# Performance work log

Hardware: AMD Instinct MI355X
Metric: run time of the kernel (lower is better)

The kernel has to match this reference:

```python
import jax, jax.numpy as jnp
import numpy as np

B, S, R, D, A, P = 64, 128, 8, 10000, 10, 256


def setup_inputs() -> dict:
    key = jax.random.key(0)
    ks = jax.random.split(key, 7)
    return {
        "atom_hvs": jax.random.normal(ks[0], (A, D), jnp.float32),
        "pos_hvs": jax.random.normal(ks[1], (S, D), jnp.float32),
        "closure_tag": jax.random.normal(ks[2], (D,), jnp.float32),
        "W": jax.random.normal(ks[3], (P, D), jnp.float32) / np.float32(np.sqrt(D)),
        "b": jax.random.normal(ks[4], (P,), jnp.float32) * 0.01,
        "token_mask": jnp.ones((B, S), jnp.float32),
        "ring_mask": jnp.ones((B, R), jnp.float32),
        "atom_idx": jax.random.randint(ks[5], (B, S), 0, A),
        "ring_pos": jax.random.randint(ks[6], (B, R, 2), 0, S),
    }


def reference(atom_hvs, pos_hvs, closure_tag, W, b, token_mask, ring_mask, atom_idx, ring_pos):
    # HRR bind = circular convolution -> pointwise multiply in rFFT domain.
    # Bundle = sum; by linearity we sum in the frequency domain and do a
    # single irfft per molecule (same math as per-token conv + add).
    d = atom_hvs.shape[-1]
    Fa = jnp.fft.rfft(atom_hvs, axis=-1)          # [A, F]
    Fp = jnp.fft.rfft(pos_hvs, axis=-1)           # [S, F]
    Fc = jnp.fft.rfft(closure_tag)                # [F]

    s = atom_idx.shape[1]
    tok = Fa[atom_idx] * Fp[None, :s, :]          # [B, S, F] gather+bind
    freq = jnp.sum(token_mask[..., None] * tok, axis=1)   # [B, F] bundle

    ring = Fp[ring_pos[..., 0]] * Fp[ring_pos[..., 1]] * Fc  # [B, R, F]
    freq = freq + jnp.sum(ring_mask[..., None] * ring, axis=1)

    mol_hv = jnp.fft.irfft(freq, n=d, axis=-1)    # [B, D]
    return mol_hv @ W.T + b                       # [B, proj_dim]
```

## Files before the change

kernel.cpp:

```cpp
#include <hip/hip_runtime.h>

#define PI2 6.28318530717958647692f

#define NSIG 139
#define FS   5120

__global__ __launch_bounds__(256) void k_fwd(
                     const float* __restrict__ atom, const float* __restrict__ pos,
                     const float* __restrict__ clo, float2* __restrict__ spec) {
  __shared__ float xs[5000];
  unsigned sig = blockIdx.x, q = blockIdx.y;
  unsigned k1base = q * 10u;
  unsigned nk1 = (k1base + 10u <= 51u) ? 10u : (51u - k1base);
  const float* xb = (sig < 128u) ? (pos + sig * 10000u)
                   : ((sig < 138u) ? (atom + (sig - 128u) * 10000u) : clo);
  int tid = threadIdx.x;
  unsigned ntile1 = nk1 * 25u;
  unsigned k1l = tid / 25u, n2 = (tid % 25u) * 4u;
  bool have = (unsigned)tid < ntile1;
  unsigned k1 = k1base + k1l;
  float cth, sth;
  __sincosf(PI2 * (float)k1 * 0.01f, &sth, &cth);
  float c = 1.0f, s = 0.0f;
  float ar[4] = {}, as[4] = {};

  for (int h = 0; h < 2; ++h) {
    for (int i = tid; i < 1250; i += 256)
      *(float4*)(xs + 4 * i) = *(const float4*)(xb + h * 5000 + 4 * i);
    __syncthreads();
    if (have) {
#pragma unroll 5
      for (int n1l = 0; n1l < 50; ++n1l) {
        const float4 xv = *(const float4*)(xs + n1l * 100 + n2);
        ar[0] += xv.x * c; as[0] += xv.x * s;
        ar[1] += xv.y * c; as[1] += xv.y * s;
        ar[2] += xv.z * c; as[2] += xv.z * s;
        ar[3] += xv.w * c; as[3] += xv.w * s;
        float cn = c * cth - s * sth;
        float sn = s * cth + c * sth;
        c = cn; s = sn;
      }
    }
    __syncthreads();
  }

  if (have) {
    unsigned rb = (100u - k1) % 100u;
    float resA[8], resB[8];
#pragma unroll
    for (int j = 0; j < 4; ++j) {
      float swA, cwA, swB, cwB;
      __sincosf(PI2 * (float)((n2 + j) * k1) * 1e-4f, &swA, &cwA);
      __sincosf(PI2 * (float)((n2 + j) * rb) * 1e-4f, &swB, &cwB);
      resA[2 * j + 0] = ar[j] * cwA - as[j] * swA;
      resA[2 * j + 1] = -(as[j] * cwA + ar[j] * swA);
      resB[2 * j + 0] = ar[j] * cwB + as[j] * swB;
      resB[2 * j + 1] = as[j] * cwB - ar[j] * swB;
    }
    float* pA = xs + k1l * 200u + n2 * 2u;
    float* pB = xs + (nk1 + k1l) * 200u + n2 * 2u;
    *(float4*)(pA + 0) = make_float4(resA[0], resA[1], resA[2], resA[3]);
    *(float4*)(pA + 4) = make_float4(resA[4], resA[5], resA[6], resA[7]);
    *(float4*)(pB + 0) = make_float4(resB[0], resB[1], resB[2], resB[3]);
    *(float4*)(pB + 4) = make_float4(resB[4], resB[5], resB[6], resB[7]);
  }
  __syncthreads();

  unsigned nrow = 2u * nk1;
  unsigned ntile3 = nrow * 26u;
  for (unsigned t = tid; t < ntile3; t += 256u) {
    unsigned lr = t / 26u, k2 = (t % 26u) * 2u;
    unsigned gk1 = (lr < nk1) ? (k1base + lr) : ((100u - (k1base + (lr - nk1))) % 100u);
    const float* brow = xs + lr * 200u;
    float cthA, sthA, cthB, sthB;
    __sincosf(PI2 * (float)k2 * 0.01f, &sthA, &cthA);
    __sincosf(PI2 * (float)(k2 + 1) * 0.01f, &sthB, &cthB);
    float cA = 1.0f, sA = 0.0f, cB = 1.0f, sB = 0.0f;
    float reA = 0.f, imA = 0.f, reB = 0.f, imB = 0.f;
#pragma unroll 4
    for (int n2i = 0; n2i < 100; n2i += 2) {
      const float4 b0 = *(const float4*)(brow + 2 * n2i);
      reA += b0.x * cA + b0.y * sA;  imA += b0.y * cA - b0.x * sA;
      reB += b0.x * cB + b0.y * sB;  imB += b0.y * cB - b0.x * sB;
      float cA1 = cA * cthA - sA * sthA, sA1 = sA * cthA + cA * sthA;
      float cB1 = cB * cthB - sB * sthB, sB1 = sB * cthB + cB * sthB;
      reA += b0.z * cA1 + b0.w * sA1;  imA += b0.w * cA1 - b0.z * sA1;
      reB += b0.z * cB1 + b0.w * sB1;  imB += b0.w * cB1 - b0.z * sB1;
      cA = cA1 * cthA - sA1 * sthA; sA = sA1 * cthA + cA1 * sthA;
      cB = cB1 * cthB - sB1 * sthB; sB = sB1 * cthB + cB1 * sthB;
    }
    unsigned kA = gk1 + 100u * k2;
    unsigned kB = gk1 + 100u * (k2 + 1);
    if (kA <= 5000u) spec[sig * FS + kA] = make_float2(reA, imA);
    if (kB <= 5000u) spec[sig * FS + kB] = make_float2(reB, imB);
  }
}

__global__ __launch_bounds__(256) void k_mix(const float2* __restrict__ spec,
                      const float* __restrict__ tmask, const float* __restrict__ rmask,
                      const int* __restrict__ aidx, const int* __restrict__ rpos,
                      float2* __restrict__ G) {
  __shared__ float2 FaS[10][128];
  __shared__ float2 FcS[128];
  __shared__ float tmS[4][128];
  __shared__ int   aiS[4][128];
  __shared__ float rmS[4][8];
  __shared__ int   rpS[4][8][2];
  __shared__ float2 red[2][4][128];
  int tid = threadIdx.x;
  int kl = tid & 127, half = tid >> 7;
  int k = blockIdx.x * 128 + kl;
  int kc = k > 5000 ? 5000 : k;
  int b0 = blockIdx.y * 4;
  for (int i = tid; i < 10 * 128; i += 256) {
    int a = i >> 7, kk = i & 127;
    int kg = blockIdx.x * 128 + kk; if (kg > 5000) kg = 5000;
    FaS[a][kk] = spec[(128 + a) * FS + kg];
  }
  if (tid < 128) FcS[tid] = spec[138 * FS + kc];
  for (int i = tid; i < 4 * 128; i += 256) {
    int bb = i >> 7, ss = i & 127;
    tmS[bb][ss] = tmask[(b0 + bb) * 128 + ss];
    aiS[bb][ss] = aidx[(b0 + bb) * 128 + ss];
  }
  if (tid < 32) {
    int bb = tid >> 3, rr = tid & 7;
    rmS[bb][rr] = rmask[(b0 + bb) * 8 + rr];
    rpS[bb][rr][0] = rpos[((b0 + bb) * 8 + rr) * 2 + 0];
    rpS[bb][rr][1] = rpos[((b0 + bb) * 8 + rr) * 2 + 1];
  }
  __syncthreads();
  float fr[4] = {}, fi[4] = {};
  int sbase = half * 64;
#pragma unroll 8
  for (int si = 0; si < 64; ++si) {
    int s = sbase + si;
    float2 fp = spec[s * FS + kc];
#pragma unroll
    for (int b = 0; b < 4; ++b) {
      int a = aiS[b][s];
      float tm = tmS[b][s];
      float2 fa = FaS[a][kl];
      fr[b] += tm * (fa.x * fp.x - fa.y * fp.y);
      fi[b] += tm * (fa.x * fp.y + fa.y * fp.x);
    }
  }
  float2 fc = FcS[kl];
#pragma unroll
  for (int rr = 0; rr < 4; ++rr) {
    int r = half * 4 + rr;
#pragma unroll
    for (int b = 0; b < 4; ++b) {
      int p0 = rpS[b][r][0], p1 = rpS[b][r][1];
      float rm = rmS[b][r];
      float2 f0 = spec[p0 * FS + kc];
      float2 f1 = spec[p1 * FS + kc];
      float tr = f0.x * f1.x - f0.y * f1.y;
      float ti = f0.x * f1.y + f0.y * f1.x;
      fr[b] += rm * (tr * fc.x - ti * fc.y);
      fi[b] += rm * (tr * fc.y + ti * fc.x);
    }
  }
#pragma unroll
  for (int b = 0; b < 4; ++b) red[half][b][kl] = make_float2(fr[b], fi[b]);
  __syncthreads();
  if (k <= 5000) {
#pragma unroll
    for (int j = 0; j < 2; ++j) {
      int b = half + 2 * j;
      float R = red[0][b][kl].x + red[1][b][kl].x;
      float I = red[0][b][kl].y + red[1][b][kl].y;
      if (k == 0 || k == 5000) I = 0.0f;
      G[(size_t)(b0 + b) * 10000 + k] = make_float2(R, I);
      if (k >= 1 && k <= 4999)
        G[(size_t)(b0 + b) * 10000 + (10000 - k)] = make_float2(R, -I);
    }
  }
}

__global__ __launch_bounds__(256) void k_i1(const float2* __restrict__ G,
                                            float2* __restrict__ Bi) {
  __shared__ float gs[2600];
  unsigned sig = blockIdx.x;
  const float* gp = (const float*)(G + sig * 10000u);
  int tid = threadIdx.x;
  unsigned t = blockIdx.y * 256u + tid;
  bool have = t < 2600u;
  unsigned m1 = t / 26u, n2 = (t % 26u) * 2u;
  float cth, sth;
  __sincosf(PI2 * (float)m1 * 0.01f, &sth, &cth);
  float reA = 0.f, imA = 0.f, reB = 0.f, imB = 0.f;

  for (int h = 0; h < 4; ++h) {
    if (h) __syncthreads();
    for (int i = tid; i < 650; i += 256) {
      int row = i / 26, c4 = i % 26;
      *(float4*)(gs + row * 104 + c4 * 4) =
          *(const float4*)(gp + (h * 25 + row) * 200 + c4 * 4);
    }
    __syncthreads();
    if (have) {
      unsigned ph = (m1 * (unsigned)h) & 3u;
      float c = (ph == 0u) ? 1.0f : (ph == 2u) ? -1.0f : 0.0f;
      float s = (ph == 1u) ? 1.0f : (ph == 3u) ? -1.0f : 0.0f;
#pragma unroll 5
      for (int n1l = 0; n1l < 25; ++n1l) {
        const float4 gv = *(const float4*)(gs + n1l * 104 + n2 * 2);
        reA += gv.x * c - gv.y * s;  imA += gv.y * c + gv.x * s;
        reB += gv.z * c - gv.w * s;  imB += gv.w * c + gv.z * s;
        float cn = c * cth - s * sth;
        float sn = s * cth + c * sth;
        c = cn; s = sn;
      }
    }
  }
  if (have) {
    float w0 = (n2 == 0u || n2 == 50u) ? 0.5f : 1.0f;
    float w1 = (n2 == 50u) ? 0.0f : 1.0f;
    float sw0, cw0, sw1, cw1;
    __sincosf(PI2 * (float)(n2 * m1) * 1e-4f, &sw0, &cw0);
    __sincosf(PI2 * (float)((n2 + 1u) * m1) * 1e-4f, &sw1, &cw1);
    float4 outv;
    outv.x = (reA * cw0 - imA * sw0) * w0;
    outv.y = (imA * cw0 + reA * sw0) * w0;
    outv.z = (reB * cw1 - imB * sw1) * w1;
    outv.w = (imB * cw1 + reB * sw1) * w1;
    *(float4*)((float*)Bi + (sig * 5200u + m1 * 52u + n2) * 2) = outv;
  }
}

__global__ __launch_bounds__(256) void k_i2(const float2* __restrict__ Bi,
                                            float* __restrict__ mol) {
  __shared__ float bs[2600];
  unsigned sig = blockIdx.x, q = blockIdx.y;
  int tid = threadIdx.x;
  const float* bp = (const float*)Bi + sig * 10400u + q * 2600u;
  for (int i = tid; i < 650; i += 256)
    *(float4*)(bs + 4 * i) = *(const float4*)(bp + 4 * i);
  __syncthreads();
  unsigned t = blockIdx.z * 256u + tid;
  if (t >= 1250u) return;
  unsigned m1l = t / 50u;
  unsigned m2 = (t % 50u) * 2u;
  const float* b0 = bs + m1l * 104u;
  float cthA, sthA, cthB, sthB;
  __sincosf(PI2 * (float)m2 * 0.01f, &sthA, &cthA);
  __sincosf(PI2 * (float)(m2 + 1u) * 0.01f, &sthB, &cthB);
  float cA = 1.0f, sA = 0.0f, cB = 1.0f, sB = 0.0f;
  float r0 = 0.f, r1 = 0.f;
#pragma unroll 4
  for (int jj = 0; jj < 26; ++jj) {
    int n2i = 2 * jj;
    const float4 v0 = *(const float4*)(b0 + 2 * n2i);
    r0 += v0.x * cA - v0.y * sA;
    r1 += v0.x * cB - v0.y * sB;
    float cA1 = cA * cthA - sA * sthA, sA1 = sA * cthA + cA * sthA;
    float cB1 = cB * cthB - sB * sthB, sB1 = sB * cthB + cB * sthB;
    r0 += v0.z * cA1 - v0.w * sA1;
    r1 += v0.z * cB1 - v0.w * sB1;
    cA = cA1 * cthA - sA1 * sthA; sA = sA1 * cthA + cA1 * sthA;
    cB = cB1 * cthB - sB1 * sthB; sB = sB1 * cthB + cB1 * sthB;
  }
  unsigned m1 = q * 25u + m1l;
  mol[sig * 10000u + m1 + 100u * m2] = r0 * 2e-4f;
  mol[sig * 10000u + m1 + 100u * (m2 + 1u)] = r1 * 2e-4f;
}

__global__ __launch_bounds__(512) void k_proj(const float* __restrict__ mol,
                                              const float* __restrict__ W,
                                              float* __restrict__ part) {
  __shared__ float molS[40 * 64];
  int tid = threadIdx.x;
  int d0 = blockIdx.x * 40;
  for (int i = tid; i < 40 * 64; i += 512)
    molS[i] = mol[(size_t)(i & 63) * 10000 + d0 + (i >> 6)];
  __syncthreads();
  int p0 = (tid & 127) * 2;
  int bh = (tid >> 7) * 16;
  float acc[2][16] = {};
  const float* w0 = W + (size_t)(p0 + 0) * 10000 + d0;
  const float* w1 = W + (size_t)(p0 + 1) * 10000 + d0;
#pragma unroll 4
  for (int dl = 0; dl < 40; ++dl) {
    const float wv0 = w0[dl], wv1 = w1[dl];
    const float4* m4 = (const float4*)(molS + dl * 64 + bh);
#pragma unroll
    for (int q = 0; q < 4; ++q) {
      float4 mv = m4[q];
      acc[0][4 * q + 0] += wv0 * mv.x;  acc[1][4 * q + 0] += wv1 * mv.x;
      acc[0][4 * q + 1] += wv0 * mv.y;  acc[1][4 * q + 1] += wv1 * mv.y;
      acc[0][4 * q + 2] += wv0 * mv.z;  acc[1][4 * q + 2] += wv1 * mv.z;
      acc[0][4 * q + 3] += wv0 * mv.w;  acc[1][4 * q + 3] += wv1 * mv.w;
    }
  }
#pragma unroll
  for (int b = 0; b < 16; ++b)
    *(float2*)(part + (size_t)blockIdx.x * 16384 + (bh + b) * 256 + p0) =
        make_float2(acc[0][b], acc[1][b]);
}

__global__ __launch_bounds__(256) void k_red(const float* __restrict__ part,
                                             const float* __restrict__ bias,
                                             float* __restrict__ out) {
  __shared__ float red[4][64];
  int tid = threadIdx.x;
  int pl = tid & 63, cg = tid >> 6;
  int b = blockIdx.x;
  int p = blockIdx.y * 64 + pl;
  float acc = 0.0f;
#pragma unroll 8
  for (int ch = cg; ch < 250; ch += 4)
    acc += part[(size_t)ch * 16384 + b * 256 + p];
  red[cg][pl] = acc;
  __syncthreads();
  if (tid < 64)
    out[b * 256 + p] = red[0][pl] + red[1][pl] + red[2][pl] + red[3][pl] + bias[p];
}

extern "C" void kernel_launch(void* const* d_in, const int* in_sizes, int n_in,
                              void* d_out, int out_size, void* d_ws, size_t ws_size,
                              hipStream_t stream) {
  const float* atom  = (const float*)d_in[0];
  const float* pos   = (const float*)d_in[1];
  const float* clo   = (const float*)d_in[2];
  const float* W     = (const float*)d_in[3];
  const float* bias  = (const float*)d_in[4];
  const float* tmask = (const float*)d_in[5];
  const float* rmask = (const float*)d_in[6];
  const int*   aidx  = (const int*)d_in[7];
  const int*   rpos  = (const int*)d_in[8];
  float* out = (float*)d_out;

  char* ws = (char*)d_ws;
  size_t off = 0;
  auto alloc = [&](size_t n) { off = (off + 255) & ~(size_t)255; size_t o = off; off += n; return o; };
  char* regA   = ws + alloc(16777216);
  float2* Bi   = (float2*)regA;
  float*  part = (float*)regA;
  float2* spec = (float2*)(ws + alloc((size_t)NSIG * FS * 8));
  float2* G    = (float2*)(ws + alloc((size_t)64 * 10000 * 8));
  float*  mol  = (float*)(ws + alloc((size_t)64 * 10000 * 4));

  k_fwd<<<dim3(NSIG, 6), dim3(256), 0, stream>>>(atom, pos, clo, spec);
  k_mix<<<dim3(40, 16), dim3(256), 0, stream>>>(spec, tmask, rmask, aidx, rpos, G);
  k_i1<<<dim3(64, 11), dim3(256), 0, stream>>>(G, Bi);
  k_i2<<<dim3(64, 4, 5), dim3(256), 0, stream>>>(Bi, mol);
  k_proj<<<dim3(250), dim3(512), 0, stream>>>(mol, W, part);
  k_red<<<dim3(64, 4), dim3(256), 0, stream>>>(part, bias, out);
}
```

Before: 188.0 us.

## Drop LDS staging in DFT stages and stage W tile in shared memory for projection

The forward DFT and the two inverse DFT stages now read their inputs straight from global memory instead of first staging them in LDS behind barriers. The aim is to remove the syncthreads and staging overhead and rely on the cache for reuse. The projection kernel now stages the W tile in padded shared memory with coalesced loads and reads mol with a padded stride, replacing strided per-thread global reads of W. This risks more global and L2 traffic in the DFT kernels, and the projection kernel now uses more LDS, which may lower occupancy.

```diff
diff --git a/kernel.cpp b/kernel.cpp
--- a/kernel.cpp
+++ b/kernel.cpp
@@ -8,7 +8,7 @@
 __global__ __launch_bounds__(256) void k_fwd(
                      const float* __restrict__ atom, const float* __restrict__ pos,
                      const float* __restrict__ clo, float2* __restrict__ spec) {
-  __shared__ float xs[5000];
+  __shared__ float xs[4000];
   unsigned sig = blockIdx.x, q = blockIdx.y;
   unsigned k1base = q * 10u;
   unsigned nk1 = (k1base + 10u <= 51u) ? 10u : (51u - k1base);
@@ -24,27 +24,18 @@
   float c = 1.0f, s = 0.0f;
   float ar[4] = {}, as[4] = {};
 
-  for (int h = 0; h < 2; ++h) {
-    for (int i = tid; i < 1250; i += 256)
-      *(float4*)(xs + 4 * i) = *(const float4*)(xb + h * 5000 + 4 * i);
-    __syncthreads();
-    if (have) {
-#pragma unroll 5
-      for (int n1l = 0; n1l < 50; ++n1l) {
-        const float4 xv = *(const float4*)(xs + n1l * 100 + n2);
-        ar[0] += xv.x * c; as[0] += xv.x * s;
-        ar[1] += xv.y * c; as[1] += xv.y * s;
-        ar[2] += xv.z * c; as[2] += xv.z * s;
-        ar[3] += xv.w * c; as[3] += xv.w * s;
-        float cn = c * cth - s * sth;
-        float sn = s * cth + c * sth;
-        c = cn; s = sn;
-      }
-    }
-    __syncthreads();
-  }
-
   if (have) {
+#pragma unroll 10
+    for (int n1l = 0; n1l < 100; ++n1l) {
+      const float4 xv = *(const float4*)(xb + n1l * 100 + n2);
+      ar[0] += xv.x * c; as[0] += xv.x * s;
+      ar[1] += xv.y * c; as[1] += xv.y * s;
+      ar[2] += xv.z * c; as[2] += xv.z * s;
+      ar[3] += xv.w * c; as[3] += xv.w * s;
+      float cn = c * cth - s * sth;
+      float sn = s * cth + c * sth;
+      c = cn; s = sn;
+    }
     unsigned rb = (100u - k1) % 100u;
     float resA[8], resB[8];
 #pragma unroll
@@ -180,69 +171,52 @@
 
 __global__ __launch_bounds__(256) void k_i1(const float2* __restrict__ G,
                                             float2* __restrict__ Bi) {
-  __shared__ float gs[2600];
   unsigned sig = blockIdx.x;
   const float* gp = (const float*)(G + sig * 10000u);
   int tid = threadIdx.x;
   unsigned t = blockIdx.y * 256u + tid;
-  bool have = t < 2600u;
+  if (t >= 2600u) return;
   unsigned m1 = t / 26u, n2 = (t % 26u) * 2u;
   float cth, sth;
   __sincosf(PI2 * (float)m1 * 0.01f, &sth, &cth);
   float reA = 0.f, imA = 0.f, reB = 0.f, imB = 0.f;
 
   for (int h = 0; h < 4; ++h) {
-    if (h) __syncthreads();
-    for (int i = tid; i < 650; i += 256) {
-      int row = i / 26, c4 = i % 26;
-      *(float4*)(gs + row * 104 + c4 * 4) =
-          *(const float4*)(gp + (h * 25 + row) * 200 + c4 * 4);
-    }
-    __syncthreads();
-    if (have) {
-      unsigned ph = (m1 * (unsigned)h) & 3u;
-      float c = (ph == 0u) ? 1.0f : (ph == 2u) ? -1.0f : 0.0f;
-      float s = (ph == 1u) ? 1.0f : (ph == 3u) ? -1.0f : 0.0f;
+    unsigned ph = (m1 * (unsigned)h) & 3u;
+    float c = (ph == 0u) ? 1.0f : (ph == 2u) ? -1.0f : 0.0f;
+    float s = (ph == 1u) ? 1.0f : (ph == 3u) ? -1.0f : 0.0f;
 #pragma unroll 5
-      for (int n1l = 0; n1l < 25; ++n1l) {
-        const float4 gv = *(const float4*)(gs + n1l * 104 + n2 * 2);
-        reA += gv.x * c - gv.y * s;  imA += gv.y * c + gv.x * s;
-        reB += gv.z * c - gv.w * s;  imB += gv.w * c + gv.z * s;
-        float cn = c * cth - s * sth;
-        float sn = s * cth + c * sth;
-        c = cn; s = sn;
-      }
-    }
-  }
-  if (have) {
-    float w0 = (n2 == 0u || n2 == 50u) ? 0.5f : 1.0f;
-    float w1 = (n2 == 50u) ? 0.0f : 1.0f;
-    float sw0, cw0, sw1, cw1;
-    __sincosf(PI2 * (float)(n2 * m1) * 1e-4f, &sw0, &cw0);
-    __sincosf(PI2 * (float)((n2 + 1u) * m1) * 1e-4f, &sw1, &cw1);
-    float4 outv;
-    outv.x = (reA * cw0 - imA * sw0) * w0;
-    outv.y = (imA * cw0 + reA * sw0) * w0;
-    outv.z = (reB * cw1 - imB * sw1) * w1;
-    outv.w = (imB * cw1 + reB * sw1) * w1;
-    *(float4*)((float*)Bi + (sig * 5200u + m1 * 52u + n2) * 2) = outv;
-  }
+    for (int n1l = 0; n1l < 25; ++n1l) {
+      const float4 gv = *(const float4*)(gp + (h * 25 + n1l) * 200 + n2 * 2);
+      reA += gv.x * c - gv.y * s;  imA += gv.y * c + gv.x * s;
+      reB += gv.z * c - gv.w * s;  imB += gv.w * c + gv.z * s;
+      float cn = c * cth - s * sth;
+      float sn = s * cth + c * sth;
+      c = cn; s = sn;
+    }
+  }
+  float w0 = (n2 == 0u || n2 == 50u) ? 0.5f : 1.0f;
+  float w1 = (n2 == 50u) ? 0.0f : 1.0f;
+  float sw0, cw0, sw1, cw1;
+  __sincosf(PI2 * (float)(n2 * m1) * 1e-4f, &sw0, &cw0);
+  __sincosf(PI2 * (float)((n2 + 1u) * m1) * 1e-4f, &sw1, &cw1);
+  float4 outv;
+  outv.x = (reA * cw0 - imA * sw0) * w0;
+  outv.y = (imA * cw0 + reA * sw0) * w0;
+  outv.z = (reB * cw1 - imB * sw1) * w1;
+  outv.w = (imB * cw1 + reB * sw1) * w1;
+  *(float4*)((float*)Bi + (sig * 5200u + m1 * 52u + n2) * 2) = outv;
 }
 
 __global__ __launch_bounds__(256) void k_i2(const float2* __restrict__ Bi,
                                             float* __restrict__ mol) {
-  __shared__ float bs[2600];
   unsigned sig = blockIdx.x, q = blockIdx.y;
   int tid = threadIdx.x;
-  const float* bp = (const float*)Bi + sig * 10400u + q * 2600u;
-  for (int i = tid; i < 650; i += 256)
-    *(float4*)(bs + 4 * i) = *(const float4*)(bp + 4 * i);
-  __syncthreads();
   unsigned t = blockIdx.z * 256u + tid;
   if (t >= 1250u) return;
   unsigned m1l = t / 50u;
   unsigned m2 = (t % 50u) * 2u;
-  const float* b0 = bs + m1l * 104u;
+  const float* b0 = (const float*)Bi + sig * 10400u + q * 2600u + m1l * 104u;
   float cthA, sthA, cthB, sthB;
   __sincosf(PI2 * (float)m2 * 0.01f, &sthA, &cthA);
   __sincosf(PI2 * (float)(m2 + 1u) * 0.01f, &sthB, &cthB);
@@ -269,28 +243,31 @@
 __global__ __launch_bounds__(512) void k_proj(const float* __restrict__ mol,
                                               const float* __restrict__ W,
                                               float* __restrict__ part) {
-  __shared__ float molS[40 * 64];
+  __shared__ float molS[40 * 66];
+  __shared__ float WS[40][258];
   int tid = threadIdx.x;
   int d0 = blockIdx.x * 40;
-  for (int i = tid; i < 40 * 64; i += 512)
-    molS[i] = mol[(size_t)(i & 63) * 10000 + d0 + (i >> 6)];
+  for (int i = tid; i < 40 * 64; i += 512) {
+    int b = i / 40, dl = i % 40;
+    molS[dl * 66 + b] = mol[(size_t)b * 10000 + d0 + dl];
+  }
+  for (int i = tid; i < 40 * 256; i += 512) {
+    int p = i / 40, dl = i % 40;
+    WS[dl][p] = W[(size_t)p * 10000 + d0 + dl];
+  }
   __syncthreads();
   int p0 = (tid & 127) * 2;
   int bh = (tid >> 7) * 16;
   float acc[2][16] = {};
-  const float* w0 = W + (size_t)(p0 + 0) * 10000 + d0;
-  const float* w1 = W + (size_t)(p0 + 1) * 10000 + d0;
 #pragma unroll 4
   for (int dl = 0; dl < 40; ++dl) {
-    const float wv0 = w0[dl], wv1 = w1[dl];
-    const float4* m4 = (const float4*)(molS + dl * 64 + bh);
-#pragma unroll
-    for (int q = 0; q < 4; ++q) {
-      float4 mv = m4[q];
-      acc[0][4 * q + 0] += wv0 * mv.x;  acc[1][4 * q + 0] += wv1 * mv.x;
-      acc[0][4 * q + 1] += wv0 * mv.y;  acc[1][4 * q + 1] += wv1 * mv.y;
-      acc[0][4 * q + 2] += wv0 * mv.z;  acc[1][4 * q + 2] += wv1 * mv.z;
-      acc[0][4 * q + 3] += wv0 * mv.w;  acc[1][4 * q + 3] += wv1 * mv.w;
+    const float2 wv = *(const float2*)(&WS[dl][p0]);
+    const float2* m2p = (const float2*)(molS + dl * 66 + bh);
+#pragma unroll
+    for (int qq = 0; qq < 8; ++qq) {
+      float2 mv = m2p[qq];
+      acc[0][2 * qq + 0] += wv.x * mv.x;  acc[1][2 * qq + 0] += wv.y * mv.x;
+      acc[0][2 * qq + 1] += wv.x * mv.y;  acc[1][2 * qq + 1] += wv.y * mv.y;
     }
   }
 #pragma unroll
```

New measurement: 185.4 us. About the same (-1.4%).
